# Kernel optimization log

Hardware: AMD Instinct MI355X
Metric: run time of the kernel (lower is better)

Reference implementation:

```python
import jax, jax.numpy as jnp
import numpy as np

D_STATE = 512
D_MODEL = 512
BATCH = 8
SEQ = 4096
DT_MIN, DT_MAX = 1e-3, 0.1
LN_EPS = 1e-5


def setup_inputs() -> dict:
    key = jax.random.key(0)
    ks = jax.random.split(key, 4)
    x = jax.random.normal(ks[0], (BATCH, SEQ, D_MODEL), dtype=jnp.float32)
    volatility_scale = jax.random.uniform(ks[1], (BATCH, SEQ, 1), dtype=jnp.float32)
    # parameters (mirroring the torch module's __init__)
    log_lambda_real = jnp.linspace(np.log(DT_MIN), np.log(DT_MAX), D_STATE).astype(jnp.float32)
    log_b = jax.random.uniform(ks[2], (D_STATE, 1), dtype=jnp.float32, minval=-0.5, maxval=0.5)
    c = jax.random.normal(ks[3], (1, D_STATE), dtype=jnp.float32) / np.sqrt(D_STATE)
    log_d = jnp.zeros((1,), jnp.float32)
    ts = np.array([1.0 / 24.0, 1.0, 5.0, 21.0, 63.0], np.float32)
    extra = np.linspace(63.0, 189.0, D_STATE - len(ts), dtype=np.float32)
    log_step = jnp.log(jnp.asarray(np.concatenate([ts, extra])))
    volatility_gate = jnp.ones((D_MODEL,), jnp.float32)
    alpha = jnp.asarray(0.7, jnp.float32)
    ln_weight = jnp.ones((D_STATE,), jnp.float32)
    ln_bias = jnp.zeros((D_STATE,), jnp.float32)
    return dict(x=x, volatility_scale=volatility_scale,
                log_lambda_real=log_lambda_real, log_b=log_b, c=c, log_d=log_d,
                log_step=log_step, volatility_gate=volatility_gate, alpha=alpha,
                ln_weight=ln_weight, ln_bias=ln_bias)


def reference(x, volatility_scale, log_lambda_real, log_b, c, log_d,
              log_step, volatility_gate, alpha, ln_weight, ln_bias):
    lam = -jnp.exp(log_lambda_real)              # [N], negative real poles
    step = jnp.exp(log_step)                     # [N], per-state timescale
    b = jnp.exp(log_b)[:, 0]                     # [N]
    d = jnp.exp(log_d)                           # [1], skip gain
    # bilinear (Tustin) discretization, paired per state
    z = step * lam                               # [N]
    a_disc = (2.0 + z) / (2.0 - z)               # [N]
    b_disc = step * (1.0 + a_disc) * b / 2.0     # [N]
    gate = jax.nn.sigmoid(volatility_gate)       # [D]
    c_vec = c[0]                                 # [N]

    def layer_norm(h):
        mu = jnp.mean(h, axis=-1, keepdims=True)
        var = jnp.var(h, axis=-1, keepdims=True)
        return (h - mu) * jax.lax.rsqrt(var + LN_EPS) * ln_weight + ln_bias

    def scan_step(h, inp):
        x_t, v_t = inp                           # [B,D], [B,1]
        h = a_disc * h + b_disc * x_t            # diagonal SSM update, [B,N]
        h = layer_norm(h)
        h = h / (1.0 + gate * v_t)               # volatility gating
        y_t = jnp.sum(h * c_vec, axis=-1, keepdims=True) + d * x_t  # [B,D]
        return h, y_t

    h0 = jnp.zeros((x.shape[0], a_disc.shape[0]), x.dtype)
    xs = (jnp.swapaxes(x, 0, 1), jnp.swapaxes(volatility_scale, 0, 1))  # time-major
    _, ys = jax.lax.scan(scan_step, h0, xs)      # [S,B,D]
    y = jnp.swapaxes(ys, 0, 1)                   # [B,S,D]
    al = jax.nn.sigmoid(alpha)
    return al * x + (1.0 - al) * y
```

## Files before the change

### kernel.cpp

```cpp
#include <hip/hip_runtime.h>
#include <cstdint>
#include <cstddef>

#define BATCH 8
#define SEQ   4096
#define DS    512
#define JPL   8
#define BLK   8
#define NBLK  (SEQ / BLK)
#define LN_EPS 1e-5f

typedef float v2f __attribute__((ext_vector_type(2)));
typedef float v4f __attribute__((ext_vector_type(4)));

static __device__ __forceinline__ v2f lo2(v4f x) { return __builtin_shufflevector(x, x, 0, 1); }
static __device__ __forceinline__ v2f hi2(v4f x) { return __builtin_shufflevector(x, x, 2, 3); }

template <int CTRL>
__device__ __forceinline__ float dpp_add(float v) {
  int t = __builtin_amdgcn_update_dpp(0, __builtin_bit_cast(int, v), CTRL, 0xF, 0xF, true);
  return v + __builtin_bit_cast(float, t);
}
__device__ __forceinline__ float wave_sum64(float v) {
  v = dpp_add<0x111>(v);
  v = dpp_add<0x112>(v);
  v = dpp_add<0x114>(v);
  v = dpp_add<0x118>(v);
  v = dpp_add<0x142>(v);
  v = dpp_add<0x143>(v);
  return v;
}
__device__ __forceinline__ float bcast63(float v) {
  return __builtin_bit_cast(float, __builtin_amdgcn_readlane(__builtin_bit_cast(int, v), 63));
}

__device__ __forceinline__ void ld16(const float* g, float* l) {
  __builtin_amdgcn_global_load_lds(
      (const __attribute__((address_space(1))) void*)g,
      (__attribute__((address_space(3))) void*)l, 16, 0, 0);
}

__global__ __launch_bounds__(192, 1) void ssm_scan(
    const float* __restrict__ x, const float* __restrict__ vol,
    const float* __restrict__ llr, const float* __restrict__ logb,
    const float* __restrict__ cvec, const float* __restrict__ lstp,
    const float* __restrict__ vgat, const float* __restrict__ lnw,
    const float* __restrict__ lnb, const float* __restrict__ alph,
    const float* __restrict__ logd, float* __restrict__ out)
{
  __shared__ __attribute__((aligned(16))) float X0[4096], X1[4096];
  __shared__ __attribute__((aligned(16))) float R0[4096], R1[4096];
  __shared__ __attribute__((aligned(16))) float SC0[512], SC1[512];
  __shared__ __attribute__((aligned(16))) float SB0[512], SB1[512];

  const int b    = blockIdx.x;
  const int lane = threadIdx.x & 63;
  const int wid  = threadIdx.x >> 6;

  if (wid == 1) {
    const float* xg = x + (size_t)b * SEQ * DS + lane * JPL;
    float* ob = out + (size_t)b * SEQ * DS;
    float al   = 1.0f / (1.0f + expf(-alph[0]));
    float dd   = expf(logd[0]);
    float coef = __builtin_fmaf(1.0f - al, dd, al);
    float c1   = 1.0f - al;

    auto dma_blk = [&](int blk, float* Xs) {
#pragma unroll
      for (int u = 0; u < BLK; ++u) {
        const float* row = xg + (size_t)(blk * BLK + u) * DS;
        ld16(row,     Xs + u * 512);
        ld16(row + 4, Xs + u * 512 + 256);
      }
    };
    auto out_blk = [&](const float* SCs, const float* Xs, int blk) {
#pragma unroll
      for (int u = 0; u < BLK; ++u) {
        float s  = bcast63(wave_sum64(SCs[u * 64 + lane]));
        float sc = c1 * s;
        v4f xa = *(const v4f*)(Xs + u * 512 + lane * 4);
        v4f xb = *(const v4f*)(Xs + u * 512 + 256 + lane * 4);
        v4f ya = xa * coef + sc;
        v4f yb = xb * coef + sc;
        float* row = ob + (size_t)(blk * BLK + u) * DS + lane * 8;
        *(v4f*)(row)     = ya;
        *(v4f*)(row + 4) = yb;
      }
    };

    dma_blk(0, X0);
    __syncthreads();
#pragma unroll 1
    for (int i2 = 0; i2 < NBLK; i2 += 2) {
      if (i2 > 0) {
        out_blk(SC1, X1, i2 - 1);
        asm volatile("s_waitcnt lgkmcnt(0)" ::: "memory");
        __builtin_amdgcn_sched_barrier(0);
      }
      dma_blk(i2 + 1, X1);
      __syncthreads();
      out_blk(SC0, X0, i2);
      if (i2 + 2 < NBLK) {
        asm volatile("s_waitcnt lgkmcnt(0)" ::: "memory");
        __builtin_amdgcn_sched_barrier(0);
        dma_blk(i2 + 2, X0);
      }
      __syncthreads();
    }
    out_blk(SC1, X1, NBLK - 1);
  } else if (wid == 2) {
    v2f gate[4];
#pragma unroll
    for (int j = 0; j < JPL; ++j)
      gate[j >> 1][j & 1] = 1.0f / (1.0f + expf(-vgat[lane * JPL + j]));
    v4f cb0, cb1;
#pragma unroll
    for (int m = 0; m < 4; ++m) {
      int n0 = lane * JPL + m, n1 = lane * JPL + 4 + m;
      cb0[m] = cvec[n0] * lnb[n0];
      cb1[m] = cvec[n1] * lnb[n1];
    }
    const float* vg = vol + (size_t)b * SEQ;

    auto rg_blk = [&](v4f Va, v4f Vb, float* Rs, float* SBs) {
#pragma unroll
      for (int u = 0; u < BLK; ++u) {
        float vt = (u < 4) ? Va[u] : Vb[u - 4];
        v4f r0, r1;
#pragma unroll
        for (int k = 0; k < 4; ++k) {
          v2f den = gate[k] * vt + 1.0f;
          float q0 = __builtin_amdgcn_rcpf(den.x);
          float q1 = __builtin_amdgcn_rcpf(den.y);
          if (k < 2) { r0[2 * k] = q0; r0[2 * k + 1] = q1; }
          else       { r1[2 * (k - 2)] = q0; r1[2 * (k - 2) + 1] = q1; }
        }
        *(v4f*)(Rs + u * 512 + lane * 4)       = r0;
        *(v4f*)(Rs + u * 512 + 256 + lane * 4) = r1;
        v4f md = cb0 * r0;
        md = __builtin_elementwise_fma(cb1, r1, md);
        v2f mh = lo2(md) + hi2(md);
        SBs[u * 64 + lane] = mh.x + mh.y;
      }
    };

    v4f V0a = *(const v4f*)(vg + 0), V0b = *(const v4f*)(vg + 4);
    v4f V1a = *(const v4f*)(vg + 8), V1b = *(const v4f*)(vg + 12);
    rg_blk(V0a, V0b, R0, SB0);
    __syncthreads();
#pragma unroll 1
    for (int i2 = 0; i2 < NBLK; i2 += 2) {
      if (i2 + 2 < NBLK) {
        V0a = *(const v4f*)(vg + (i2 + 2) * BLK);
        V0b = *(const v4f*)(vg + (i2 + 2) * BLK + 4);
      }
      rg_blk(V1a, V1b, R1, SB1);
      __syncthreads();
      if (i2 + 3 < NBLK) {
        V1a = *(const v4f*)(vg + (i2 + 3) * BLK);
        V1b = *(const v4f*)(vg + (i2 + 3) * BLK + 4);
      }
      if (i2 + 2 < NBLK) rg_blk(V0a, V0b, R0, SB0);
      __syncthreads();
    }
  } else {
    v2f bd[4], aw[4], ab[4], cw[4];
#pragma unroll
    for (int j = 0; j < JPL; ++j) {
      int n = lane * JPL + j;
      float lam = -expf(llr[n]);
      float st  = expf(lstp[n]);
      float z   = st * lam;
      float ad  = (2.0f + z) / (2.0f - z);
      float bdv = st * (1.0f + ad) * expf(logb[n]) * 0.5f;
      float wv  = lnw[n], bi = lnb[n], cv = cvec[n];
      bd[j >> 1][j & 1] = bdv;
      aw[j >> 1][j & 1] = ad * wv;
      ab[j >> 1][j & 1] = ad * bi;
      cw[j >> 1][j & 1] = cv * wv;
    }
    v2f hp[4];
#pragma unroll
    for (int k = 0; k < 4; ++k) hp[k] = (v2f){0.0f, 0.0f};

    auto proc_blk = [&](const float* Xs, const float* Rs, const float* SBs, float* SCs) {
#pragma unroll
      for (int u = 0; u < BLK; ++u) {
        v4f xx0 = *(const v4f*)(Xs + u * 512 + lane * 4);
        v4f xx1 = *(const v4f*)(Xs + u * 512 + 256 + lane * 4);
        v4f rr0 = *(const v4f*)(Rs + u * 512 + lane * 4);
        v4f rr1 = *(const v4f*)(Rs + u * 512 + 256 + lane * 4);
        float u3s = SBs[u * 64 + lane];
        v2f xs[4] = {lo2(xx0), hi2(xx0), lo2(xx1), hi2(xx1)};
        v2f rs[4] = {lo2(rr0), hi2(rr0), lo2(rr1), hi2(rr1)};

        v2f hr[4], q[4], abrs[4];
#pragma unroll
        for (int k = 0; k < 4; ++k) {
          hr[k]   = __builtin_elementwise_fma(bd[k], xs[k], hp[k]);
          q[k]    = rs[k] * hr[k];
          abrs[k] = ab[k] * rs[k];
        }
        v2f t01 = hr[0] + hr[1], t23 = hr[2] + hr[3];
        v2f tt  = t01 + t23;
        float s1 = tt.x + tt.y;
        v2f m01 = hr[0] * hr[0];
        m01 = __builtin_elementwise_fma(hr[1], hr[1], m01);
        v2f m23 = hr[2] * hr[2];
        m23 = __builtin_elementwise_fma(hr[3], hr[3], m23);
        v2f mm = m01 + m23;
        float s2 = mm.x + mm.y;

        s1 = bcast63(wave_sum64(s1));
        s2 = bcast63(wave_sum64(s2));
        float mu  = s1 * (1.0f / DS);
        float m2e = __builtin_fmaf(s2, 1.0f / DS, LN_EPS);
        float var = __builtin_fmaf(-mu, mu, m2e);
        float inv = __builtin_amdgcn_rsqf(var);

        v2f muv = {mu, mu}, invv = {inv, inv};
        v2f tv[4];
#pragma unroll
        for (int k = 0; k < 4; ++k)
          tv[k] = __builtin_elementwise_fma(-muv, rs[k], q[k]);
#pragma unroll
        for (int k = 0; k < 4; ++k) {
          v2f sv = aw[k] * tv[k];
          hp[k]  = __builtin_elementwise_fma(invv, sv, abrs[k]);
        }
        v2f u0 = cw[0] * tv[0];
        u0 = __builtin_elementwise_fma(cw[1], tv[1], u0);
        v2f u2 = cw[2] * tv[2];
        u2 = __builtin_elementwise_fma(cw[3], tv[3], u2);
        v2f uu = u0 + u2;
        float u1s = uu.x + uu.y;
        SCs[u * 64 + lane] = __builtin_fmaf(inv, u1s, u3s);
      }
    };

    __syncthreads();
#pragma unroll 1
    for (int i2 = 0; i2 < NBLK; i2 += 2) {
      proc_blk(X0, R0, SB0, SC0);
      __syncthreads();
      proc_blk(X1, R1, SB1, SC1);
      __syncthreads();
    }
  }
}

extern "C" void kernel_launch(void* const* d_in, const int* in_sizes, int n_in,
                              void* d_out, int out_size, void* d_ws, size_t ws_size,
                              hipStream_t stream) {
  const float* x    = (const float*)d_in[0];
  const float* vol  = (const float*)d_in[1];
  const float* llr  = (const float*)d_in[2];
  const float* logb = (const float*)d_in[3];
  const float* cvec = (const float*)d_in[4];
  const float* logd = (const float*)d_in[5];
  const float* lstp = (const float*)d_in[6];
  const float* vgat = (const float*)d_in[7];
  const float* alph = (const float*)d_in[8];
  const float* lnw  = (const float*)d_in[9];
  const float* lnb  = (const float*)d_in[10];
  float* outf = (float*)d_out;

  ssm_scan<<<BATCH, 192, 0, stream>>>(x, vol, llr, logb, cvec, lstp,
                                      vgat, lnw, lnb, alph, logd, outf);
}
```

Baseline: 676.2 us.

## Move output writeback to gating wave and deepen x prefetch to four buffers

Wave 1 now only issues asynchronous global-to-LDS loads of x, two blocks ahead into a four-slot ring buffer. The output epilogue (wave reduction of SC, blend with x, global stores) moves to wave 2, which also computes the volatility gating factors. This is meant to keep the x DMA from stalling behind store traffic and to give the loads more lead time ahead of the scan wave. It costs extra LDS and adds the store work to wave 2's critical path, and the buffer reuse depends on the barrier-count ordering being correct.

```diff
diff --git a/kernel.cpp b/kernel.cpp
--- a/kernel.cpp
+++ b/kernel.cpp
@@ -48,7 +48,7 @@
     const float* __restrict__ lnb, const float* __restrict__ alph,
     const float* __restrict__ logd, float* __restrict__ out)
 {
-  __shared__ __attribute__((aligned(16))) float X0[4096], X1[4096];
+  __shared__ __attribute__((aligned(16))) float X[4][4096];
   __shared__ __attribute__((aligned(16))) float R0[4096], R1[4096];
   __shared__ __attribute__((aligned(16))) float SC0[512], SC1[512];
   __shared__ __attribute__((aligned(16))) float SB0[512], SB1[512];
@@ -59,68 +59,41 @@
 
   if (wid == 1) {
     const float* xg = x + (size_t)b * SEQ * DS + lane * JPL;
-    float* ob = out + (size_t)b * SEQ * DS;
+    auto dma_blk = [&](int blk) {
+      float* Xs = X[blk & 3];
+#pragma unroll
+      for (int u = 0; u < BLK; ++u) {
+        const float* row = xg + (size_t)(blk * BLK + u) * DS;
+        ld16(row,     Xs + u * 512);
+        ld16(row + 4, Xs + u * 512 + 256);
+      }
+    };
+    dma_blk(0);
+    dma_blk(1);
+    __syncthreads();
+#pragma unroll 1
+    for (int i = 0; i < NBLK; ++i) {
+      if (i + 2 < NBLK) dma_blk(i + 2);
+      __syncthreads();
+    }
+  } else if (wid == 2) {
+    v2f gate[4];
+#pragma unroll
+    for (int j = 0; j < JPL; ++j)
+      gate[j >> 1][j & 1] = 1.0f / (1.0f + expf(-vgat[lane * JPL + j]));
+    v4f cb0, cb1;
+#pragma unroll
+    for (int m = 0; m < 4; ++m) {
+      int n0 = lane * JPL + m, n1 = lane * JPL + 4 + m;
+      cb0[m] = cvec[n0] * lnb[n0];
+      cb1[m] = cvec[n1] * lnb[n1];
+    }
     float al   = 1.0f / (1.0f + expf(-alph[0]));
     float dd   = expf(logd[0]);
     float coef = __builtin_fmaf(1.0f - al, dd, al);
     float c1   = 1.0f - al;
-
-    auto dma_blk = [&](int blk, float* Xs) {
-#pragma unroll
-      for (int u = 0; u < BLK; ++u) {
-        const float* row = xg + (size_t)(blk * BLK + u) * DS;
-        ld16(row,     Xs + u * 512);
-        ld16(row + 4, Xs + u * 512 + 256);
-      }
-    };
-    auto out_blk = [&](const float* SCs, const float* Xs, int blk) {
-#pragma unroll
-      for (int u = 0; u < BLK; ++u) {
-        float s  = bcast63(wave_sum64(SCs[u * 64 + lane]));
-        float sc = c1 * s;
-        v4f xa = *(const v4f*)(Xs + u * 512 + lane * 4);
-        v4f xb = *(const v4f*)(Xs + u * 512 + 256 + lane * 4);
-        v4f ya = xa * coef + sc;
-        v4f yb = xb * coef + sc;
-        float* row = ob + (size_t)(blk * BLK + u) * DS + lane * 8;
-        *(v4f*)(row)     = ya;
-        *(v4f*)(row + 4) = yb;
-      }
-    };
-
-    dma_blk(0, X0);
-    __syncthreads();
-#pragma unroll 1
-    for (int i2 = 0; i2 < NBLK; i2 += 2) {
-      if (i2 > 0) {
-        out_blk(SC1, X1, i2 - 1);
-        asm volatile("s_waitcnt lgkmcnt(0)" ::: "memory");
-        __builtin_amdgcn_sched_barrier(0);
-      }
-      dma_blk(i2 + 1, X1);
-      __syncthreads();
-      out_blk(SC0, X0, i2);
-      if (i2 + 2 < NBLK) {
-        asm volatile("s_waitcnt lgkmcnt(0)" ::: "memory");
-        __builtin_amdgcn_sched_barrier(0);
-        dma_blk(i2 + 2, X0);
-      }
-      __syncthreads();
-    }
-    out_blk(SC1, X1, NBLK - 1);
-  } else if (wid == 2) {
-    v2f gate[4];
-#pragma unroll
-    for (int j = 0; j < JPL; ++j)
-      gate[j >> 1][j & 1] = 1.0f / (1.0f + expf(-vgat[lane * JPL + j]));
-    v4f cb0, cb1;
-#pragma unroll
-    for (int m = 0; m < 4; ++m) {
-      int n0 = lane * JPL + m, n1 = lane * JPL + 4 + m;
-      cb0[m] = cvec[n0] * lnb[n0];
-      cb1[m] = cvec[n1] * lnb[n1];
-    }
     const float* vg = vol + (size_t)b * SEQ;
+    float* ob = out + (size_t)b * SEQ * DS;
 
     auto rg_blk = [&](v4f Va, v4f Vb, float* Rs, float* SBs) {
 #pragma unroll
@@ -143,26 +116,41 @@
         SBs[u * 64 + lane] = mh.x + mh.y;
       }
     };
-
-    v4f V0a = *(const v4f*)(vg + 0), V0b = *(const v4f*)(vg + 4);
-    v4f V1a = *(const v4f*)(vg + 8), V1b = *(const v4f*)(vg + 12);
-    rg_blk(V0a, V0b, R0, SB0);
+    auto out_blk = [&](int blk) {
+      const float* SCs = (blk & 1) ? SC1 : SC0;
+      const float* Xs  = X[blk & 3];
+#pragma unroll
+      for (int u = 0; u < BLK; ++u) {
+        float s  = bcast63(wave_sum64(SCs[u * 64 + lane]));
+        float sc = c1 * s;
+        v4f xa = *(const v4f*)(Xs + u * 512 + lane * 4);
+        v4f xb = *(const v4f*)(Xs + u * 512 + 256 + lane * 4);
+        float* row = ob + (size_t)(blk * BLK + u) * DS + lane * 8;
+        *(v4f*)(row)     = xa * coef + sc;
+        *(v4f*)(row + 4) = xb * coef + sc;
+      }
+    };
+
+    {
+      v4f V0a = *(const v4f*)(vg + 0), V0b = *(const v4f*)(vg + 4);
+      rg_blk(V0a, V0b, R0, SB0);
+    }
+    v4f Va_ = *(const v4f*)(vg + 1 * BLK), Vb_ = *(const v4f*)(vg + 1 * BLK + 4);
+    v4f Na_ = *(const v4f*)(vg + 2 * BLK), Nb_ = *(const v4f*)(vg + 2 * BLK + 4);
     __syncthreads();
 #pragma unroll 1
-    for (int i2 = 0; i2 < NBLK; i2 += 2) {
-      if (i2 + 2 < NBLK) {
-        V0a = *(const v4f*)(vg + (i2 + 2) * BLK);
-        V0b = *(const v4f*)(vg + (i2 + 2) * BLK + 4);
-      }
-      rg_blk(V1a, V1b, R1, SB1);
+    for (int i = 0; i < NBLK; ++i) {
+      if (i >= 1) out_blk(i - 1);
+      if (i + 1 < NBLK)
+        rg_blk(Va_, Vb_, (i & 1) ? R0 : R1, (i & 1) ? SB0 : SB1);
+      Va_ = Na_; Vb_ = Nb_;
+      if (i + 3 < NBLK) {
+        Na_ = *(const v4f*)(vg + (i + 3) * BLK);
+        Nb_ = *(const v4f*)(vg + (i + 3) * BLK + 4);
+      }
       __syncthreads();
-      if (i2 + 3 < NBLK) {
-        V1a = *(const v4f*)(vg + (i2 + 3) * BLK);
-        V1b = *(const v4f*)(vg + (i2 + 3) * BLK + 4);
-      }
-      if (i2 + 2 < NBLK) rg_blk(V0a, V0b, R0, SB0);
-      __syncthreads();
-    }
+    }
+    out_blk(NBLK - 1);
   } else {
     v2f bd[4], aw[4], ab[4], cw[4];
 #pragma unroll
@@ -240,10 +228,9 @@
 
     __syncthreads();
 #pragma unroll 1
-    for (int i2 = 0; i2 < NBLK; i2 += 2) {
-      proc_blk(X0, R0, SB0, SC0);
-      __syncthreads();
-      proc_blk(X1, R1, SB1, SC1);
+    for (int i = 0; i < NBLK; ++i) {
+      proc_blk(X[i & 3], (i & 1) ? R1 : R0,
+               (i & 1) ? SB1 : SB0, (i & 1) ? SC1 : SC0);
       __syncthreads();
     }
   }
```

Measured after the change: 1.003 ms. 48.3% more time.
